# Kernel optimization log

Measured on AMD Instinct MI355X. Metric: run time of the kernel, lower is better.

The kernel has to match this reference:

```python
import jax, jax.numpy as jnp
import numpy as np

B, S, D = 4, 4096, 200


def setup_inputs() -> dict:
    key = jax.random.key(0)
    ks = jax.random.split(key, 10)
    sc = 1.0 / np.sqrt(D)
    return {
        "modal1_input": jax.random.normal(ks[0], (B, S, D), dtype=jnp.float32),
        "modal2_input": jax.random.normal(ks[1], (B, S, D), dtype=jnp.float32),
        "Wq": jax.random.normal(ks[2], (D, D), dtype=jnp.float32) * sc,
        "bq": jnp.zeros((D,), dtype=jnp.float32),
        "Wk": jax.random.normal(ks[3], (D, D), dtype=jnp.float32) * sc,
        "bk": jnp.zeros((D,), dtype=jnp.float32),
        "Wv": jax.random.normal(ks[4], (D, D), dtype=jnp.float32) * sc,
        "bv": jnp.zeros((D,), dtype=jnp.float32),
        "Wo": jax.random.normal(ks[5], (D, D), dtype=jnp.float32) * sc,
        "bo": jnp.zeros((D,), dtype=jnp.float32),
    }


def _self_attend(x, Wq, bq, Wk, bk, Wv, bv):
    # torch nn.Linear: y = x @ W.T + b
    q = x @ Wq.T + bq  # [B,S,D]
    k = x @ Wk.T + bk
    v = x @ Wv.T + bv
    scale = 1.0 / jnp.sqrt(jnp.asarray(q.shape[-1], q.dtype))
    scores = jnp.einsum("bsd,btd->bst", q, k) * scale  # [B,S,S]
    w = jax.nn.softmax(scores, axis=-1)
    return jnp.einsum("bst,btd->bsd", w, v)


def reference(modal1_input, modal2_input, Wq, bq, Wk, bk, Wv, bv, Wo, bo):
    a1 = _self_attend(modal1_input, Wq, bq, Wk, bk, Wv, bv)
    a2 = _self_attend(modal2_input, Wq, bq, Wk, bk, Wv, bv)
    fused = a1 + a2
    return fused @ Wo.T + bo
```

## Files before the change

kernel.cpp:

```cpp
#include <hip/hip_runtime.h>

#define SLEN 4096
#define DIM  200
#define DP   224
#define DPL  232
#define VD   208
#define VTL  72

typedef __bf16 bf16t;
typedef bf16t bf16x8 __attribute__((ext_vector_type(8)));
typedef float f32x4 __attribute__((ext_vector_type(4)));

static __device__ __forceinline__ f32x4 mfma16(bf16x8 a, bf16x8 b, f32x4 c) {
    return __builtin_amdgcn_mfma_f32_16x16x32_bf16(a, b, c, 0, 0, 0);
}

static __device__ __forceinline__ unsigned short f2bf(float f) {
    unsigned int u = __float_as_uint(f);
    u += 0x7FFFu + ((u >> 16) & 1u);
    return (unsigned short)(u >> 16);
}

static __device__ __forceinline__ uint2 pack4(float a, float b, float c, float d) {
    uint2 r;
    r.x = (unsigned)f2bf(a) | ((unsigned)f2bf(b) << 16);
    r.y = (unsigned)f2bf(c) | ((unsigned)f2bf(d) << 16);
    return r;
}

__global__ __launch_bounds__(256, 2)
void proj_kernel(const float* __restrict__ x1, const float* __restrict__ x2,
                 const float* __restrict__ Wq, const float* __restrict__ bq,
                 const float* __restrict__ Wk, const float* __restrict__ bk,
                 const float* __restrict__ Wv, const float* __restrict__ bv,
                 unsigned short* __restrict__ Qg, unsigned short* __restrict__ Kg,
                 unsigned short* __restrict__ Vtg)
{
    __shared__ unsigned short x_lds[64 * DPL];
    __shared__ unsigned short w_lds[64 * DPL];
    __shared__ unsigned short vt_lds[64 * 66];

    const int tid = threadIdx.x;
    const int mod = blockIdx.x >> 8;
    const int rb  = blockIdx.x & 255;
    const int r0  = rb * 64;
    const int bidx = r0 >> 12;
    const int s0  = r0 & 4095;
    const int unit = mod * 4 + bidx;
    const float* __restrict__ x = mod ? x2 : x1;

    for (int i = tid; i < 3200; i += 256) {
        int r = i / 50, c = i % 50;
        const float4 v = *(const float4*)(x + (size_t)(r0 + r) * DIM + c * 4);
        *(uint2*)(x_lds + r * DPL + c * 4) = pack4(v.x, v.y, v.z, v.w);
    }
    {
        int r = tid >> 2, c4 = tid & 3;
        uint2 z = make_uint2(0u, 0u);
        *(uint2*)(x_lds + r * DPL + 200 + c4 * 4) = z;
        *(uint2*)(x_lds + r * DPL + 216 + c4 * 4) = z;
        *(uint2*)(w_lds + r * DPL + 200 + c4 * 4) = z;
        *(uint2*)(w_lds + r * DPL + 216 + c4 * 4) = z;
    }
    __syncthreads();

    const int wv = tid >> 6, lane = tid & 63, ln = lane & 15, h = lane >> 4;

    bf16x8 afrag[7];
    #pragma unroll
    for (int kk = 0; kk < 7; ++kk)
        afrag[kk] = *(const bf16x8*)(x_lds + (wv * 16 + ln) * DPL + kk * 32 + 8 * h);

    for (int mmat = 0; mmat < 3; ++mmat) {
        const float* W  = (mmat == 0) ? Wq : (mmat == 1 ? Wk : Wv);
        const float* bi = (mmat == 0) ? bq : (mmat == 1 ? bk : bv);
        for (int t = 0; t < 4; ++t) {
            for (int i = tid; i < 3200; i += 256) {
                int r = i / 50, c = i % 50;
                int og = t * 64 + r;
                uint2 val = make_uint2(0u, 0u);
                if (og < DIM) {
                    const float4 v = *(const float4*)(W + (size_t)og * DIM + c * 4);
                    val = pack4(v.x, v.y, v.z, v.w);
                }
                *(uint2*)(w_lds + r * DPL + c * 4) = val;
            }
            __syncthreads();

            f32x4 acc[4];
            #pragma unroll
            for (int sub = 0; sub < 4; ++sub) acc[sub] = (f32x4){0.f, 0.f, 0.f, 0.f};
            #pragma unroll
            for (int kk = 0; kk < 7; ++kk) {
                #pragma unroll
                for (int sub = 0; sub < 4; ++sub) {
                    bf16x8 bfrag = *(const bf16x8*)(w_lds + (sub * 16 + ln) * DPL + kk * 32 + 8 * h);
                    acc[sub] = mfma16(afrag[kk], bfrag, acc[sub]);
                }
            }

            if (mmat < 2) {
                unsigned short* dst = (mmat == 0) ? Qg : Kg;
                #pragma unroll
                for (int sub = 0; sub < 4; ++sub) {
                    int og = t * 64 + sub * 16 + ln;
                    if (og < DIM) {
                        float bias = bi[og];
                        #pragma unroll
                        for (int r = 0; r < 4; ++r) {
                            int srow = s0 + wv * 16 + 4 * h + r;
                            dst[((size_t)unit * SLEN + srow) * DP + og] = f2bf(acc[sub][r] + bias);
                        }
                    }
                }
                __syncthreads();
            } else {
                #pragma unroll
                for (int sub = 0; sub < 4; ++sub) {
                    int og = t * 64 + sub * 16 + ln;
                    float bias = (og < DIM) ? bi[og] : 0.f;
                    #pragma unroll
                    for (int r = 0; r < 4; ++r) {
                        float val = (og < DIM) ? (acc[sub][r] + bias) : 0.f;
                        vt_lds[(wv * 16 + 4 * h + r) * 66 + sub * 16 + ln] = f2bf(val);
                    }
                }
                __syncthreads();
                for (int p = 0; p < 2; ++p) {
                    int idx = p * 256 + tid;
                    int dl = idx >> 3, cc = idx & 7;
                    int og = t * 64 + dl;
                    if (og < VD) {
                        unsigned short tmp[8];
                        #pragma unroll
                        for (int j = 0; j < 8; ++j)
                            tmp[j] = vt_lds[(cc * 8 + j) * 66 + dl];
                        *(uint4*)(Vtg + ((size_t)unit * VD + og) * SLEN + s0 + cc * 8) = *(uint4*)tmp;
                    }
                }
                __syncthreads();
            }
        }
    }
}

__global__ __launch_bounds__(512, 2)
void attn_kernel(const unsigned short* __restrict__ Qg,
                 const unsigned short* __restrict__ Kg,
                 const unsigned short* __restrict__ Vtg,
                 float* __restrict__ Og)
{
    __shared__ unsigned short k_lds[64 * DPL];
    __shared__ unsigned short vt_lds[VD * VTL];
    __shared__ unsigned short p_lds[8 * 16 * VTL];

    const int tid = threadIdx.x;
    const int u   = blockIdx.x & 7;
    const int qt  = blockIdx.x >> 3;
    const int wv = tid >> 6, lane = tid & 63, ln = lane & 15, h = lane >> 4;
    const size_t ubase = (size_t)u * SLEN;

    bf16x8 qfrag[7];
    {
        const size_t qoff = (ubase + qt * 128 + wv * 16 + ln) * DP;
        #pragma unroll
        for (int kk = 0; kk < 7; ++kk)
            qfrag[kk] = *(const bf16x8*)(Qg + qoff + kk * 32 + 8 * h);
    }

    float mrun[4], lrun[4];
    #pragma unroll
    for (int r = 0; r < 4; ++r) { mrun[r] = -1e30f; lrun[r] = 0.f; }
    f32x4 acc[13];
    #pragma unroll
    for (int d = 0; d < 13; ++d) acc[d] = (f32x4){0.f, 0.f, 0.f, 0.f};

    const float scale = 0.07071067811865475f;

    for (int t0 = 0; t0 < SLEN; t0 += 64) {
        #pragma unroll
        for (int it = 0; it < 4; ++it) {
            int i = it * 512 + tid;
            if (i < 1792) {
                int r = i / 28, c = i % 28;
                *(uint4*)(k_lds + r * DPL + c * 8) =
                    *(const uint4*)(Kg + (ubase + t0 + r) * DP + c * 8);
            }
            if (i < 1664) {
                int r = i >> 3, c = i & 7;
                *(uint4*)(vt_lds + r * VTL + c * 8) =
                    *(const uint4*)(Vtg + ((size_t)u * VD + r) * SLEN + t0 + c * 8);
            }
        }
        __syncthreads();

        f32x4 sc[4];
        #pragma unroll
        for (int sub = 0; sub < 4; ++sub) sc[sub] = (f32x4){0.f, 0.f, 0.f, 0.f};
        #pragma unroll
        for (int kk = 0; kk < 7; ++kk) {
            #pragma unroll
            for (int sub = 0; sub < 4; ++sub) {
                bf16x8 bfrag = *(const bf16x8*)(k_lds + (sub * 16 + ln) * DPL + kk * 32 + 8 * h);
                sc[sub] = mfma16(qfrag[kk], bfrag, sc[sub]);
            }
        }

        #pragma unroll
        for (int r = 0; r < 4; ++r) {
            float mx = fmaxf(fmaxf(sc[0][r], sc[1][r]), fmaxf(sc[2][r], sc[3][r]));
            mx = fmaxf(mx, __shfl_xor(mx, 1));
            mx = fmaxf(mx, __shfl_xor(mx, 2));
            mx = fmaxf(mx, __shfl_xor(mx, 4));
            mx = fmaxf(mx, __shfl_xor(mx, 8));
            mx *= scale;
            float mnew = fmaxf(mrun[r], mx);
            float alpha = __expf(mrun[r] - mnew);
            float rsum = 0.f;
            #pragma unroll
            for (int sub = 0; sub < 4; ++sub) {
                float p = __expf(sc[sub][r] * scale - mnew);
                rsum += p;
                p_lds[wv * (16 * VTL) + (4 * h + r) * VTL + sub * 16 + ln] = f2bf(p);
            }
            rsum += __shfl_xor(rsum, 1);
            rsum += __shfl_xor(rsum, 2);
            rsum += __shfl_xor(rsum, 4);
            rsum += __shfl_xor(rsum, 8);
            lrun[r] = lrun[r] * alpha + rsum;
            mrun[r] = mnew;
            #pragma unroll
            for (int d = 0; d < 13; ++d) acc[d][r] *= alpha;
        }

        #pragma unroll
        for (int ks = 0; ks < 2; ++ks) {
            bf16x8 pfrag = *(const bf16x8*)(p_lds + wv * (16 * VTL) + ln * VTL + ks * 32 + 8 * h);
            #pragma unroll
            for (int d = 0; d < 13; ++d) {
                bf16x8 bfrag = *(const bf16x8*)(vt_lds + (d * 16 + ln) * VTL + ks * 32 + 8 * h);
                acc[d] = mfma16(pfrag, bfrag, acc[d]);
            }
        }
        __syncthreads();
    }

    #pragma unroll
    for (int r = 0; r < 4; ++r) {
        float inv = 1.f / lrun[r];
        int srow = qt * 128 + wv * 16 + 4 * h + r;
        #pragma unroll
        for (int d = 0; d < 13; ++d)
            Og[(ubase + srow) * VD + d * 16 + ln] = acc[d][r] * inv;
    }
}

__global__ __launch_bounds__(256, 2)
void out_kernel(const float* __restrict__ Og, const float* __restrict__ Wo,
                const float* __restrict__ bo, float* __restrict__ out)
{
    __shared__ unsigned short a_lds[64 * DPL];
    __shared__ unsigned short w_lds[64 * DPL];

    const int tid = threadIdx.x;
    const int r0 = blockIdx.x * 64;
    const int bidx = r0 >> 12;
    const int s0 = r0 & 4095;

    const float* O1 = Og + (size_t)(0 + bidx) * SLEN * VD;
    const float* O2 = Og + (size_t)(4 + bidx) * SLEN * VD;

    for (int i = tid; i < 3200; i += 256) {
        int r = i / 50, c = i % 50;
        size_t off = (size_t)(s0 + r) * VD + c * 4;
        float4 a = *(const float4*)(O1 + off);
        float4 b = *(const float4*)(O2 + off);
        *(uint2*)(a_lds + r * DPL + c * 4) = pack4(a.x + b.x, a.y + b.y, a.z + b.z, a.w + b.w);
    }
    {
        int r = tid >> 2, c4 = tid & 3;
        uint2 z = make_uint2(0u, 0u);
        *(uint2*)(a_lds + r * DPL + 200 + c4 * 4) = z;
        *(uint2*)(a_lds + r * DPL + 216 + c4 * 4) = z;
        *(uint2*)(w_lds + r * DPL + 200 + c4 * 4) = z;
        *(uint2*)(w_lds + r * DPL + 216 + c4 * 4) = z;
    }
    __syncthreads();

    const int wv = tid >> 6, lane = tid & 63, ln = lane & 15, h = lane >> 4;
    bf16x8 afrag[7];
    #pragma unroll
    for (int kk = 0; kk < 7; ++kk)
        afrag[kk] = *(const bf16x8*)(a_lds + (wv * 16 + ln) * DPL + kk * 32 + 8 * h);

    for (int t = 0; t < 4; ++t) {
        for (int i = tid; i < 3200; i += 256) {
            int r = i / 50, c = i % 50;
            int og = t * 64 + r;
            uint2 val = make_uint2(0u, 0u);
            if (og < DIM) {
                const float4 v = *(const float4*)(Wo + (size_t)og * DIM + c * 4);
                val = pack4(v.x, v.y, v.z, v.w);
            }
            *(uint2*)(w_lds + r * DPL + c * 4) = val;
        }
        __syncthreads();

        f32x4 acc[4];
        #pragma unroll
        for (int sub = 0; sub < 4; ++sub) acc[sub] = (f32x4){0.f, 0.f, 0.f, 0.f};
        #pragma unroll
        for (int kk = 0; kk < 7; ++kk) {
            #pragma unroll
            for (int sub = 0; sub < 4; ++sub) {
                bf16x8 bfrag = *(const bf16x8*)(w_lds + (sub * 16 + ln) * DPL + kk * 32 + 8 * h);
                acc[sub] = mfma16(afrag[kk], bfrag, acc[sub]);
            }
        }

        #pragma unroll
        for (int sub = 0; sub < 4; ++sub) {
            int og = t * 64 + sub * 16 + ln;
            if (og < DIM) {
                float bias = bo[og];
                #pragma unroll
                for (int r = 0; r < 4; ++r) {
                    int row = r0 + wv * 16 + 4 * h + r;
                    out[(size_t)row * DIM + og] = acc[sub][r] + bias;
                }
            }
        }
        __syncthreads();
    }
}

extern "C" void kernel_launch(void* const* d_in, const int* in_sizes, int n_in,
                              void* d_out, int out_size, void* d_ws, size_t ws_size,
                              hipStream_t stream)
{
    const float* x1 = (const float*)d_in[0];
    const float* x2 = (const float*)d_in[1];
    const float* Wq = (const float*)d_in[2];
    const float* bq = (const float*)d_in[3];
    const float* Wk = (const float*)d_in[4];
    const float* bk = (const float*)d_in[5];
    const float* Wv = (const float*)d_in[6];
    const float* bv = (const float*)d_in[7];
    const float* Wo = (const float*)d_in[8];
    const float* bo = (const float*)d_in[9];

    unsigned short* Qg  = (unsigned short*)d_ws;
    unsigned short* Kg  = Qg + (size_t)8 * SLEN * DP;
    unsigned short* Vtg = Kg + (size_t)8 * SLEN * DP;
    float*          Og  = (float*)(Vtg + (size_t)8 * VD * SLEN);

    proj_kernel<<<dim3(512), dim3(256), 0, stream>>>(x1, x2, Wq, bq, Wk, bk, Wv, bv,
                                                     Qg, Kg, Vtg);
    attn_kernel<<<dim3(256), dim3(512), 0, stream>>>(Qg, Kg, Vtg, Og);
    out_kernel<<<dim3(256), dim3(256), 0, stream>>>(Og, Wo, bo, (float*)d_out);
}
```

Measured before the change: 469.5 us.

## Split attention KV range in two halves and merge partials in output kernel

Splits the key/value sequence into two halves handled by separate blocks, doubling the attention grid to 512 blocks so more of the GPU's compute units are busy. Each half writes unnormalized bf16 partial outputs plus running max and sum, and the output kernel merges them with log-sum-exp weights. It also adds a lazy rescale that only updates the running max when it grows by more than 8, which skips most per-tile accumulator rescaling. The trade-offs are extra partial-output traffic, bf16 rounding of the partial sums, and a higher occupancy hint that may force register spills.

```diff
diff --git a/kernel.cpp b/kernel.cpp
--- a/kernel.cpp
+++ b/kernel.cpp
@@ -6,6 +6,7 @@
 #define DPL  232
 #define VD   208
 #define VTL  72
+#define HKV  2048
 
 typedef __bf16 bf16t;
 typedef bf16t bf16x8 __attribute__((ext_vector_type(8)));
@@ -19,6 +20,10 @@
     unsigned int u = __float_as_uint(f);
     u += 0x7FFFu + ((u >> 16) & 1u);
     return (unsigned short)(u >> 16);
+}
+
+static __device__ __forceinline__ float bf2f(unsigned short s) {
+    return __uint_as_float((unsigned)s << 16);
 }
 
 static __device__ __forceinline__ uint2 pack4(float a, float b, float c, float d) {
@@ -144,11 +149,12 @@
     }
 }
 
-__global__ __launch_bounds__(512, 2)
+__global__ __launch_bounds__(512, 4)
 void attn_kernel(const unsigned short* __restrict__ Qg,
                  const unsigned short* __restrict__ Kg,
                  const unsigned short* __restrict__ Vtg,
-                 float* __restrict__ Og)
+                 unsigned short* __restrict__ Ap,
+                 float2* __restrict__ Mlg)
 {
     __shared__ unsigned short k_lds[64 * DPL];
     __shared__ unsigned short vt_lds[VD * VTL];
@@ -156,7 +162,8 @@
 
     const int tid = threadIdx.x;
     const int u   = blockIdx.x & 7;
-    const int qt  = blockIdx.x >> 3;
+    const int qt  = (blockIdx.x >> 3) & 31;
+    const int hf  = blockIdx.x >> 8;
     const int wv = tid >> 6, lane = tid & 63, ln = lane & 15, h = lane >> 4;
     const size_t ubase = (size_t)u * SLEN;
 
@@ -176,8 +183,9 @@
     for (int d = 0; d < 13; ++d) acc[d] = (f32x4){0.f, 0.f, 0.f, 0.f};
 
     const float scale = 0.07071067811865475f;
-
-    for (int t0 = 0; t0 < SLEN; t0 += 64) {
+    const int t_beg = hf * HKV;
+
+    for (int t0 = t_beg; t0 < t_beg + HKV; t0 += 64) {
         #pragma unroll
         for (int it = 0; it < 4; ++it) {
             int i = it * 512 + tid;
@@ -206,6 +214,7 @@
             }
         }
 
+        float mxs[4];
         #pragma unroll
         for (int r = 0; r < 4; ++r) {
             float mx = fmaxf(fmaxf(sc[0][r], sc[1][r]), fmaxf(sc[2][r], sc[3][r]));
@@ -213,13 +222,29 @@
             mx = fmaxf(mx, __shfl_xor(mx, 2));
             mx = fmaxf(mx, __shfl_xor(mx, 4));
             mx = fmaxf(mx, __shfl_xor(mx, 8));
-            mx *= scale;
-            float mnew = fmaxf(mrun[r], mx);
-            float alpha = __expf(mrun[r] - mnew);
+            mxs[r] = mx * scale;
+        }
+
+        int need = (mxs[0] > mrun[0] + 8.f) | (mxs[1] > mrun[1] + 8.f) |
+                   (mxs[2] > mrun[2] + 8.f) | (mxs[3] > mrun[3] + 8.f);
+        if (__any(need)) {
+            #pragma unroll
+            for (int r = 0; r < 4; ++r) {
+                float mnew = fmaxf(mrun[r], mxs[r]);
+                float alpha = __expf(mrun[r] - mnew);
+                lrun[r] *= alpha;
+                #pragma unroll
+                for (int d = 0; d < 13; ++d) acc[d][r] *= alpha;
+                mrun[r] = mnew;
+            }
+        }
+
+        #pragma unroll
+        for (int r = 0; r < 4; ++r) {
             float rsum = 0.f;
             #pragma unroll
             for (int sub = 0; sub < 4; ++sub) {
-                float p = __expf(sc[sub][r] * scale - mnew);
+                float p = __expf(sc[sub][r] * scale - mrun[r]);
                 rsum += p;
                 p_lds[wv * (16 * VTL) + (4 * h + r) * VTL + sub * 16 + ln] = f2bf(p);
             }
@@ -227,10 +252,7 @@
             rsum += __shfl_xor(rsum, 2);
             rsum += __shfl_xor(rsum, 4);
             rsum += __shfl_xor(rsum, 8);
-            lrun[r] = lrun[r] * alpha + rsum;
-            mrun[r] = mnew;
-            #pragma unroll
-            for (int d = 0; d < 13; ++d) acc[d][r] *= alpha;
+            lrun[r] += rsum;
         }
 
         #pragma unroll
@@ -245,18 +267,23 @@
         __syncthreads();
     }
 
+    const int slab = hf * 8 + u;
+    unsigned short* Adst = Ap + (size_t)slab * SLEN * VD;
     #pragma unroll
     for (int r = 0; r < 4; ++r) {
-        float inv = 1.f / lrun[r];
         int srow = qt * 128 + wv * 16 + 4 * h + r;
         #pragma unroll
         for (int d = 0; d < 13; ++d)
-            Og[(ubase + srow) * VD + d * 16 + ln] = acc[d][r] * inv;
+            Adst[(size_t)srow * VD + d * 16 + ln] = f2bf(acc[d][r]);
+        if (ln == 0)
+            Mlg[(size_t)slab * SLEN + srow] = make_float2(mrun[r], lrun[r]);
     }
 }
 
 __global__ __launch_bounds__(256, 2)
-void out_kernel(const float* __restrict__ Og, const float* __restrict__ Wo,
+void out_kernel(const unsigned short* __restrict__ Ap,
+                const float2* __restrict__ Mlg,
+                const float* __restrict__ Wo,
                 const float* __restrict__ bo, float* __restrict__ out)
 {
     __shared__ unsigned short a_lds[64 * DPL];
@@ -267,15 +294,45 @@
     const int bidx = r0 >> 12;
     const int s0 = r0 & 4095;
 
-    const float* O1 = Og + (size_t)(0 + bidx) * SLEN * VD;
-    const float* O2 = Og + (size_t)(4 + bidx) * SLEN * VD;
+    const unsigned short* A1a = Ap + (size_t)(bidx)      * SLEN * VD;
+    const unsigned short* A1b = Ap + (size_t)(8 + bidx)  * SLEN * VD;
+    const unsigned short* A2a = Ap + (size_t)(4 + bidx)  * SLEN * VD;
+    const unsigned short* A2b = Ap + (size_t)(12 + bidx) * SLEN * VD;
+    const float2* M1a = Mlg + (size_t)(bidx)      * SLEN;
+    const float2* M1b = Mlg + (size_t)(8 + bidx)  * SLEN;
+    const float2* M2a = Mlg + (size_t)(4 + bidx)  * SLEN;
+    const float2* M2b = Mlg + (size_t)(12 + bidx) * SLEN;
 
     for (int i = tid; i < 3200; i += 256) {
         int r = i / 50, c = i % 50;
-        size_t off = (size_t)(s0 + r) * VD + c * 4;
-        float4 a = *(const float4*)(O1 + off);
-        float4 b = *(const float4*)(O2 + off);
-        *(uint2*)(a_lds + r * DPL + c * 4) = pack4(a.x + b.x, a.y + b.y, a.z + b.z, a.w + b.w);
+        int srow = s0 + r;
+        size_t off = (size_t)srow * VD + c * 4;
+
+        float2 ml1a = M1a[srow], ml1b = M1b[srow];
+        float2 ml2a = M2a[srow], ml2b = M2b[srow];
+        float M1 = fmaxf(ml1a.x, ml1b.x);
+        float w1a = __expf(ml1a.x - M1), w1b = __expf(ml1b.x - M1);
+        float inv1 = 1.f / (ml1a.y * w1a + ml1b.y * w1b);
+        float M2 = fmaxf(ml2a.x, ml2b.x);
+        float w2a = __expf(ml2a.x - M2), w2b = __expf(ml2b.x - M2);
+        float inv2 = 1.f / (ml2a.y * w2a + ml2b.y * w2b);
+
+        uint2 pa = *(const uint2*)(A1a + off);
+        uint2 pb = *(const uint2*)(A1b + off);
+        uint2 qa = *(const uint2*)(A2a + off);
+        uint2 qb = *(const uint2*)(A2b + off);
+
+        float f[4];
+        f[0] = (bf2f((unsigned short)(pa.x & 0xffff)) * w1a + bf2f((unsigned short)(pb.x & 0xffff)) * w1b) * inv1
+             + (bf2f((unsigned short)(qa.x & 0xffff)) * w2a + bf2f((unsigned short)(qb.x & 0xffff)) * w2b) * inv2;
+        f[1] = (bf2f((unsigned short)(pa.x >> 16))    * w1a + bf2f((unsigned short)(pb.x >> 16))    * w1b) * inv1
+             + (bf2f((unsigned short)(qa.x >> 16))    * w2a + bf2f((unsigned short)(qb.x >> 16))    * w2b) * inv2;
+        f[2] = (bf2f((unsigned short)(pa.y & 0xffff)) * w1a + bf2f((unsigned short)(pb.y & 0xffff)) * w1b) * inv1
+             + (bf2f((unsigned short)(qa.y & 0xffff)) * w2a + bf2f((unsigned short)(qb.y & 0xffff)) * w2b) * inv2;
+        f[3] = (bf2f((unsigned short)(pa.y >> 16))    * w1a + bf2f((unsigned short)(pb.y >> 16))    * w1b) * inv1
+             + (bf2f((unsigned short)(qa.y >> 16))    * w2a + bf2f((unsigned short)(qb.y >> 16))    * w2b) * inv2;
+
+        *(uint2*)(a_lds + r * DPL + c * 4) = pack4(f[0], f[1], f[2], f[3]);
     }
     {
         int r = tid >> 2, c4 = tid & 3;
@@ -352,10 +409,11 @@
     unsigned short* Qg  = (unsigned short*)d_ws;
     unsigned short* Kg  = Qg + (size_t)8 * SLEN * DP;
     unsigned short* Vtg = Kg + (size_t)8 * SLEN * DP;
-    float*          Og  = (float*)(Vtg + (size_t)8 * VD * SLEN);
+    unsigned short* Apg = Vtg + (size_t)8 * VD * SLEN;
+    float2*         Mlg = (float2*)(Apg + (size_t)16 * SLEN * VD);
 
     proj_kernel<<<dim3(512), dim3(256), 0, stream>>>(x1, x2, Wq, bq, Wk, bk, Wv, bv,
                                                      Qg, Kg, Vtg);
-    attn_kernel<<<dim3(256), dim3(512), 0, stream>>>(Qg, Kg, Vtg, Og);
-    out_kernel<<<dim3(256), dim3(256), 0, stream>>>(Og, Wo, bo, (float*)d_out);
-}
+    attn_kernel<<<dim3(512), dim3(512), 0, stream>>>(Qg, Kg, Vtg, Apg, Mlg);
+    out_kernel<<<dim3(256), dim3(256), 0, stream>>>(Apg, Mlg, Wo, bo, (float*)d_out);
+}
```

Measured after the change: 409.1 us. 12.9% less time.
